# Performance work log

Measured on AMD Instinct MI355X. Metric: run time of the kernel, lower is better.

Reference implementation:

```python
import jax, jax.numpy as jnp
import numpy as np

NUM_EMBEDDINGS = 1024
EMBEDDING_DIM = 64
COMMITMENT_COST = 0.25


def setup_inputs() -> dict:
    key = jax.random.key(0)
    k1, k2 = jax.random.split(key)
    z = jax.random.normal(k1, (16, EMBEDDING_DIM, 64, 64), dtype=jnp.float32)
    # nn.Embedding init: uniform(-1/K, 1/K)
    emb = jax.random.uniform(
        k2, (NUM_EMBEDDINGS, EMBEDDING_DIM), dtype=jnp.float32,
        minval=-1.0 / NUM_EMBEDDINGS, maxval=1.0 / NUM_EMBEDDINGS)
    return {"z": z, "emb": emb}


def reference(z, emb):
    # b c h w -> b h w c
    zc = jnp.transpose(z, (0, 2, 3, 1))
    B, H, W, D = zc.shape
    zf = zc.reshape(-1, D)  # [N, D]
    K = emb.shape[0]

    # L2 distances: ||z||^2 + ||e||^2 - 2 z e^T   -> [N, K]
    distances = (jnp.sum(zf * zf, axis=1, keepdims=True)
                 + jnp.sum(emb * emb, axis=1)
                 - 2.0 * jnp.matmul(zf, emb.T))
    encoding_indices = jnp.argmin(distances, axis=1)  # [N]

    # one_hot @ emb  ==  gather
    quantized = emb[encoding_indices].reshape(zc.shape)  # [B,H,W,D]

    reconstruction_errors = jnp.sum((quantized - zc) ** 2, axis=-1).reshape(-1)
    avg_error = jnp.mean(reconstruction_errors)

    e_latent_loss = jnp.mean((jax.lax.stop_gradient(quantized) - zc) ** 2)
    q_latent_loss = jnp.mean((quantized - jax.lax.stop_gradient(zc)) ** 2)
    loss = q_latent_loss + COMMITMENT_COST * e_latent_loss

    # straight-through estimator
    quantized_st = zc + jax.lax.stop_gradient(quantized - zc)
    out = jnp.transpose(quantized_st, (0, 3, 1, 2))  # b h w c -> b c h w

    # perplexity: avg one-hot usage (histogram instead of dense one-hot)
    N = zf.shape[0]
    counts = jnp.zeros((K,), dtype=jnp.float32).at[encoding_indices].add(1.0)
    avg_probs = counts / N
    perplexity = jnp.exp(-jnp.sum(avg_probs * jnp.log(avg_probs + 1e-10)))

    return out, loss, perplexity, avg_error
```

## Files before the change

### kernel.cpp

```cpp
#include <hip/hip_runtime.h>
#include <stdint.h>

#define HW   4096
#define NEMB 1024

typedef float        f32x4  __attribute__((ext_vector_type(4)));
typedef short        bf16x8 __attribute__((ext_vector_type(8)));
typedef unsigned int u32x4  __attribute__((ext_vector_type(4)));

#define CVTPK(D, LO, HI) asm("v_cvt_pk_bf16_f32 %0, %1, %2" : "=v"(D) : "v"(LO), "v"(HI))

__device__ __forceinline__ void gload_lds16(const float* g, float* l) {
    __builtin_amdgcn_global_load_lds(
        (const __attribute__((address_space(1))) void*)(uintptr_t)g,
        (__attribute__((address_space(3))) void*)(uintptr_t)l, 16, 0, 0);
}

__global__ __launch_bounds__(128) void vq_init(const float* __restrict__ emb,
                                               unsigned int* __restrict__ counts,
                                               float* __restrict__ errsum,
                                               float* __restrict__ ens) {
    const int gid  = blockIdx.x * 128 + threadIdx.x;
    const int k    = gid >> 1;
    const int half = gid & 1;
    if (half == 0) counts[k] = 0u;
    if (gid == 0) *errsum = 0.0f;
    const float* e = emb + k * 64 + half * 32;
    float nrm = 0.0f;
    #pragma unroll
    for (int c = 0; c < 4; ++c) {
        f32x4 v0 = *(const f32x4*)(e + c * 8);
        f32x4 v1 = *(const f32x4*)(e + c * 8 + 4);
        nrm += v0.x*v0.x + v0.y*v0.y + v0.z*v0.z + v0.w*v0.w
             + v1.x*v1.x + v1.y*v1.y + v1.z*v1.z + v1.w*v1.w;
    }
    float o = __shfl_xor(nrm, 1, 64);
    if (half == 0) ens[k] = 1.0f + (nrm + o);
}

__global__ __launch_bounds__(512, 4)
void vq_main(const float* __restrict__ z, const float* __restrict__ emb,
             const float* __restrict__ ens,
             float* __restrict__ out, unsigned int* __restrict__ counts,
             float* __restrict__ errsum)
{
    __shared__ __attribute__((aligned(16))) float z_lds[64 * 128];
    __shared__ __attribute__((aligned(16))) unsigned int et_w[256 * 32];
    __shared__ __attribute__((aligned(16))) float ens_lds[NEMB];
    __shared__ int   idx_sh[128];
    __shared__ float errp[512];

    const int t   = threadIdx.x;
    const int n0  = blockIdx.x * 128;
    const int bb  = n0 >> 12;
    const int hw0 = n0 & 4095;
    const float* zb = z + bb * (64 * HW) + hw0;

    #pragma unroll
    for (int it = 0; it < 4; ++it) {
        const int p = it * 512 + t;
        gload_lds16(zb + (p >> 5) * HW + (p & 31) * 4, z_lds + p * 4);
    }
    if (t < 256) gload_lds16(ens + t * 4, ens_lds + t * 4);

    #pragma unroll
    for (int it = 0; it < 4; ++it) {
        const int q = it * 512 + t;
        const int r = q >> 3, c = q & 7;
        const float* s2 = emb + r * 64 + c * 8;
        f32x4 e0 = *(const f32x4*)s2;
        f32x4 e1 = *(const f32x4*)(s2 + 4);
        u32x4 v;
        CVTPK(v.x, e0.x, e0.y); CVTPK(v.y, e0.z, e0.w);
        CVTPK(v.z, e1.x, e1.y); CVTPK(v.w, e1.z, e1.w);
        *(u32x4*)&et_w[r * 32 + ((c ^ (r & 7)) << 2)] = v;
    }
    __syncthreads();

    const int l   = t & 63;
    const int wv  = t >> 6;
    const int col = l & 15;
    const int bg  = l >> 4;

    bf16x8 a0, a1;
    {
        const int xs = wv * 16 + col;
        u32x4 wa, wb;
        #pragma unroll
        for (int p2 = 0; p2 < 4; ++p2) {
            float lo = z_lds[(bg * 8 + p2 * 2    ) * 128 + xs];
            float hi = z_lds[(bg * 8 + p2 * 2 + 1) * 128 + xs];
            CVTPK(wa[p2], lo, hi);
            float lo2 = z_lds[(32 + bg * 8 + p2 * 2    ) * 128 + xs];
            float hi2 = z_lds[(32 + bg * 8 + p2 * 2 + 1) * 128 + xs];
            CVTPK(wb[p2], lo2, hi2);
        }
        a0 = __builtin_bit_cast(bf16x8, wa);
        a1 = __builtin_bit_cast(bf16x8, wb);
    }

    const int slot0 = bg ^ (col & 7);
    const unsigned int* ep0 = et_w + col * 32 + slot0 * 4;
    const unsigned int* ep1 = et_w + col * 32 + (slot0 ^ 4) * 4;
    const float* ensp = ens_lds + col;

    unsigned int mkey[4] = {~0u, ~0u, ~0u, ~0u};

    #pragma unroll
    for (int kt = 0; kt < 4; ++kt) {
        f32x4 pf[8];
        if (kt < 3) {
            const float* src = emb + (kt + 1) * 256 * 64;
            #pragma unroll
            for (int it = 0; it < 4; ++it) {
                const int q = it * 512 + t;
                const float* s2 = src + (q >> 3) * 64 + (q & 7) * 8;
                pf[it * 2]     = *(const f32x4*)s2;
                pf[it * 2 + 1] = *(const f32x4*)(s2 + 4);
            }
        }

        __builtin_amdgcn_s_setprio(1);
        #pragma unroll
        for (int i = 0; i < 16; ++i) {
            u32x4 bw0 = *(const u32x4*)(ep0 + i * 512);
            u32x4 bw1 = *(const u32x4*)(ep1 + i * 512);
            float en1 = ensp[kt * 256 + i * 16];
            f32x4 cc = {0.0f, 0.0f, 0.0f, 0.0f};
            cc = __builtin_amdgcn_mfma_f32_16x16x32_bf16(a0, __builtin_bit_cast(bf16x8, bw0), cc, 0, 0, 0);
            cc = __builtin_amdgcn_mfma_f32_16x16x32_bf16(a1, __builtin_bit_cast(bf16x8, bw1), cc, 0, 0, 0);
            const unsigned int kg = (unsigned int)(kt * 256 + i * 16 + col);
            #pragma unroll
            for (int j = 0; j < 4; ++j) {
                float s = fmaf(-2.0f, cc[j], en1);
                unsigned int key = (__builtin_bit_cast(unsigned int, s) & 0xFFFFFC00u) | kg;
                mkey[j] = mkey[j] < key ? mkey[j] : key;
            }
        }
        __builtin_amdgcn_s_setprio(0);

        u32x4 vv[4];
        if (kt < 3) {
            #pragma unroll
            for (int it = 0; it < 4; ++it) {
                CVTPK(vv[it].x, pf[it*2].x,   pf[it*2].y);
                CVTPK(vv[it].y, pf[it*2].z,   pf[it*2].w);
                CVTPK(vv[it].z, pf[it*2+1].x, pf[it*2+1].y);
                CVTPK(vv[it].w, pf[it*2+1].z, pf[it*2+1].w);
            }
        }

        __syncthreads();
        if (kt < 3) {
            #pragma unroll
            for (int it = 0; it < 4; ++it) {
                const int q = it * 512 + t;
                const int r = q >> 3, c = q & 7;
                *(u32x4*)&et_w[r * 32 + ((c ^ (r & 7)) << 2)] = vv[it];
            }
            __syncthreads();
        }
    }

    #pragma unroll
    for (int j = 0; j < 4; ++j) {
        #pragma unroll
        for (int m = 1; m <= 8; m <<= 1) {
            unsigned int o = (unsigned int)__shfl_xor((int)mkey[j], m, 64);
            mkey[j] = mkey[j] < o ? mkey[j] : o;
        }
    }
    if (col == 0) {
        #pragma unroll
        for (int j = 0; j < 4; ++j)
            idx_sh[wv * 16 + bg * 4 + j] = (int)(mkey[j] & 1023u);
    }
    __syncthreads();

    if (t < 128) atomicAdd(&counts[idx_sh[t]], 1u);

    {
        const int x  = t & 127;
        const int cg = t >> 7;
        const int idx = idx_sh[x];
        const float* er = emb + idx * 64;
        float* ob = out + bb * (64 * HW) + hw0 + x;
        float part = 0.0f;
        #pragma unroll
        for (int cq = 0; cq < 4; ++cq) {
            const int c = cg * 16 + cq * 4;
            f32x4 e4 = *(const f32x4*)&er[c];
            float z0 = z_lds[(c+0) * 128 + x];
            float z1 = z_lds[(c+1) * 128 + x];
            float z2 = z_lds[(c+2) * 128 + x];
            float z3 = z_lds[(c+3) * 128 + x];
            ob[(c+0) * HW] = z0 + (e4.x - z0);
            ob[(c+1) * HW] = z1 + (e4.y - z1);
            ob[(c+2) * HW] = z2 + (e4.z - z2);
            ob[(c+3) * HW] = z3 + (e4.w - z3);
            float d0 = z0 - e4.x, d1 = z1 - e4.y, d2 = z2 - e4.z, d3 = z3 - e4.w;
            part = fmaf(d0, d0, part); part = fmaf(d1, d1, part);
            part = fmaf(d2, d2, part); part = fmaf(d3, d3, part);
        }
        errp[t] = part;
    }
    __syncthreads();
    if (t < 128) {
        float s = (errp[t] + errp[t + 128]) + (errp[t + 256] + errp[t + 384]);
        #pragma unroll
        for (int off = 32; off >= 1; off >>= 1) s += __shfl_down(s, off, 64);
        if ((t & 63) == 0) atomicAdd(errsum, s);
    }
}

__global__ __launch_bounds__(256) void vq_fin(const unsigned int* __restrict__ counts,
                                              const float* __restrict__ errsum,
                                              float* __restrict__ scal)
{
    __shared__ float part[4];
    const int t = threadIdx.x;
    float s = 0.0f;
    for (int k = t; k < NEMB; k += 256) {
        float p = (float)counts[k] * (1.0f / 65536.0f);
        s += p * logf(p + 1e-10f);
    }
    #pragma unroll
    for (int off = 32; off >= 1; off >>= 1) s += __shfl_down(s, off, 64);
    if ((t & 63) == 0) part[t >> 6] = s;
    __syncthreads();
    if (t == 0) {
        float tot = (part[0] + part[1]) + (part[2] + part[3]);
        float es  = *errsum;
        scal[0] = 1.25f * (es * (1.0f / 4194304.0f));
        scal[1] = expf(-tot);
        scal[2] = es * (1.0f / 65536.0f);
    }
}

extern "C" void kernel_launch(void* const* d_in, const int* in_sizes, int n_in,
                              void* d_out, int out_size, void* d_ws, size_t ws_size,
                              hipStream_t stream) {
    const float* z   = (const float*)d_in[0];
    const float* emb = (const float*)d_in[1];
    float* out = (float*)d_out;
    unsigned int* counts = (unsigned int*)d_ws;
    float* errsum = (float*)((char*)d_ws + 4096);
    float* ens    = (float*)((char*)d_ws + 8192);

    vq_init<<<16, 128, 0, stream>>>(emb, counts, errsum, ens);
    vq_main<<<512, 512, 0, stream>>>(z, emb, ens, out, counts, errsum);
    vq_fin<<<1, 256, 0, stream>>>(counts, errsum, out + 4194304);
}
```

Before: 44.55 us.

## Pre-convert codebook to swizzled bf16 once and stream it via double-buffered LDS DMA

The init kernel now converts the codebook to bf16 once, in the swizzled layout, and writes it to workspace. The main kernel then loads 128-row tiles directly into two LDS buffers with global_load_lds, double-buffered across 8 k-steps. This replaces the per-block fp32 loads, conversions and register-staged stores of all 1024 rows. It also drops one block-wide sync and the LDS stage in the error reduction, so each wave does its own shuffle reduce and atomic. The cost is more syncs per block (8 tile steps instead of 4), more atomics on errsum, and hand-written vmcnt waits that must match the number of outstanding loads.

```diff
diff --git a/kernel.cpp b/kernel.cpp
--- a/kernel.cpp
+++ b/kernel.cpp
@@ -10,7 +10,7 @@
 
 #define CVTPK(D, LO, HI) asm("v_cvt_pk_bf16_f32 %0, %1, %2" : "=v"(D) : "v"(LO), "v"(HI))
 
-__device__ __forceinline__ void gload_lds16(const float* g, float* l) {
+__device__ __forceinline__ void gload_lds16(const void* g, void* l) {
     __builtin_amdgcn_global_load_lds(
         (const __attribute__((address_space(1))) void*)(uintptr_t)g,
         (__attribute__((address_space(3))) void*)(uintptr_t)l, 16, 0, 0);
@@ -19,20 +19,27 @@
 __global__ __launch_bounds__(128) void vq_init(const float* __restrict__ emb,
                                                unsigned int* __restrict__ counts,
                                                float* __restrict__ errsum,
-                                               float* __restrict__ ens) {
+                                               float* __restrict__ ens,
+                                               unsigned int* __restrict__ embw) {
     const int gid  = blockIdx.x * 128 + threadIdx.x;
     const int k    = gid >> 1;
     const int half = gid & 1;
     if (half == 0) counts[k] = 0u;
     if (gid == 0) *errsum = 0.0f;
     const float* e = emb + k * 64 + half * 32;
+    unsigned int* dst = embw + (k >> 7) * 4096 + (k & 127) * 32;
     float nrm = 0.0f;
     #pragma unroll
-    for (int c = 0; c < 4; ++c) {
-        f32x4 v0 = *(const f32x4*)(e + c * 8);
-        f32x4 v1 = *(const f32x4*)(e + c * 8 + 4);
+    for (int ci = 0; ci < 4; ++ci) {
+        const int c = half * 4 + ci;
+        f32x4 v0 = *(const f32x4*)(e + ci * 8);
+        f32x4 v1 = *(const f32x4*)(e + ci * 8 + 4);
         nrm += v0.x*v0.x + v0.y*v0.y + v0.z*v0.z + v0.w*v0.w
              + v1.x*v1.x + v1.y*v1.y + v1.z*v1.z + v1.w*v1.w;
+        u32x4 w;
+        CVTPK(w.x, v0.x, v0.y); CVTPK(w.y, v0.z, v0.w);
+        CVTPK(w.z, v1.x, v1.y); CVTPK(w.w, v1.z, v1.w);
+        *(u32x4*)&dst[(c ^ (k & 7)) << 2] = w;
     }
     float o = __shfl_xor(nrm, 1, 64);
     if (half == 0) ens[k] = 1.0f + (nrm + o);
@@ -40,15 +47,16 @@
 
 __global__ __launch_bounds__(512, 4)
 void vq_main(const float* __restrict__ z, const float* __restrict__ emb,
-             const float* __restrict__ ens,
+             const float* __restrict__ ens, const unsigned int* __restrict__ embw,
              float* __restrict__ out, unsigned int* __restrict__ counts,
              float* __restrict__ errsum)
 {
     __shared__ __attribute__((aligned(16))) float z_lds[64 * 128];
-    __shared__ __attribute__((aligned(16))) unsigned int et_w[256 * 32];
+    __shared__ __attribute__((aligned(16))) unsigned int et0[4096];
+    __shared__ __attribute__((aligned(16))) unsigned int et1[4096];
     __shared__ __attribute__((aligned(16))) float ens_lds[NEMB];
     __shared__ int   idx_sh[128];
-    __shared__ float errp[512];
+    __shared__ float errw[8];
 
     const int t   = threadIdx.x;
     const int n0  = blockIdx.x * 128;
@@ -62,18 +70,15 @@
         gload_lds16(zb + (p >> 5) * HW + (p & 31) * 4, z_lds + p * 4);
     }
     if (t < 256) gload_lds16(ens + t * 4, ens_lds + t * 4);
-
-    #pragma unroll
-    for (int it = 0; it < 4; ++it) {
-        const int q = it * 512 + t;
-        const int r = q >> 3, c = q & 7;
-        const float* s2 = emb + r * 64 + c * 8;
-        f32x4 e0 = *(const f32x4*)s2;
-        f32x4 e1 = *(const f32x4*)(s2 + 4);
-        u32x4 v;
-        CVTPK(v.x, e0.x, e0.y); CVTPK(v.y, e0.z, e0.w);
-        CVTPK(v.z, e1.x, e1.y); CVTPK(v.w, e1.z, e1.w);
-        *(u32x4*)&et_w[r * 32 + ((c ^ (r & 7)) << 2)] = v;
+    #pragma unroll
+    for (int it = 0; it < 2; ++it) {
+        const int p = it * 512 + t;
+        gload_lds16(embw + p * 4, et0 + p * 4);
+    }
+    #pragma unroll
+    for (int it = 0; it < 2; ++it) {
+        const int p = it * 512 + t;
+        gload_lds16(embw + 4096 + p * 4, et1 + p * 4);
     }
     __syncthreads();
 
@@ -99,37 +104,27 @@
         a1 = __builtin_bit_cast(bf16x8, wb);
     }
 
-    const int slot0 = bg ^ (col & 7);
-    const unsigned int* ep0 = et_w + col * 32 + slot0 * 4;
-    const unsigned int* ep1 = et_w + col * 32 + (slot0 ^ 4) * 4;
+    const int slot0 = (bg ^ (col & 7)) << 2;
+    const int rowoff = col * 32;
     const float* ensp = ens_lds + col;
 
     unsigned int mkey[4] = {~0u, ~0u, ~0u, ~0u};
 
-    #pragma unroll
-    for (int kt = 0; kt < 4; ++kt) {
-        f32x4 pf[8];
-        if (kt < 3) {
-            const float* src = emb + (kt + 1) * 256 * 64;
-            #pragma unroll
-            for (int it = 0; it < 4; ++it) {
-                const int q = it * 512 + t;
-                const float* s2 = src + (q >> 3) * 64 + (q & 7) * 8;
-                pf[it * 2]     = *(const f32x4*)s2;
-                pf[it * 2 + 1] = *(const f32x4*)(s2 + 4);
-            }
-        }
-
-        __builtin_amdgcn_s_setprio(1);
-        #pragma unroll
-        for (int i = 0; i < 16; ++i) {
+    #pragma unroll 2
+    for (int kt = 0; kt < 8; ++kt) {
+        const unsigned int* etb = (kt & 1) ? et1 : et0;
+        const unsigned int* ep0 = etb + rowoff + slot0;
+        const unsigned int* ep1 = etb + rowoff + (slot0 ^ 16);
+
+        #pragma unroll
+        for (int i = 0; i < 8; ++i) {
             u32x4 bw0 = *(const u32x4*)(ep0 + i * 512);
             u32x4 bw1 = *(const u32x4*)(ep1 + i * 512);
-            float en1 = ensp[kt * 256 + i * 16];
+            float en1 = ensp[kt * 128 + i * 16];
             f32x4 cc = {0.0f, 0.0f, 0.0f, 0.0f};
             cc = __builtin_amdgcn_mfma_f32_16x16x32_bf16(a0, __builtin_bit_cast(bf16x8, bw0), cc, 0, 0, 0);
             cc = __builtin_amdgcn_mfma_f32_16x16x32_bf16(a1, __builtin_bit_cast(bf16x8, bw1), cc, 0, 0, 0);
-            const unsigned int kg = (unsigned int)(kt * 256 + i * 16 + col);
+            const unsigned int kg = (unsigned int)(kt * 128 + i * 16 + col);
             #pragma unroll
             for (int j = 0; j < 4; ++j) {
                 float s = fmaf(-2.0f, cc[j], en1);
@@ -137,26 +132,20 @@
                 mkey[j] = mkey[j] < key ? mkey[j] : key;
             }
         }
-        __builtin_amdgcn_s_setprio(0);
-
-        u32x4 vv[4];
-        if (kt < 3) {
-            #pragma unroll
-            for (int it = 0; it < 4; ++it) {
-                CVTPK(vv[it].x, pf[it*2].x,   pf[it*2].y);
-                CVTPK(vv[it].y, pf[it*2].z,   pf[it*2].w);
-                CVTPK(vv[it].z, pf[it*2+1].x, pf[it*2+1].y);
-                CVTPK(vv[it].w, pf[it*2+1].z, pf[it*2+1].w);
-            }
-        }
-
-        __syncthreads();
-        if (kt < 3) {
-            #pragma unroll
-            for (int it = 0; it < 4; ++it) {
-                const int q = it * 512 + t;
-                const int r = q >> 3, c = q & 7;
-                *(u32x4*)&et_w[r * 32 + ((c ^ (r & 7)) << 2)] = vv[it];
+
+        if (kt < 7) {
+            __syncthreads();
+            if (kt < 6) {
+                unsigned int* wbuf = (kt & 1) ? et1 : et0;
+                const unsigned int* src = embw + (kt + 2) * 4096;
+                #pragma unroll
+                for (int it = 0; it < 2; ++it) {
+                    const int p = it * 512 + t;
+                    gload_lds16(src + p * 4, wbuf + p * 4);
+                }
+                asm volatile("s_waitcnt vmcnt(2)" ::: "memory");
+            } else {
+                asm volatile("s_waitcnt vmcnt(0)" ::: "memory");
             }
             __syncthreads();
         }
@@ -179,13 +168,13 @@
 
     if (t < 128) atomicAdd(&counts[idx_sh[t]], 1u);
 
+    float part = 0.0f;
     {
         const int x  = t & 127;
         const int cg = t >> 7;
         const int idx = idx_sh[x];
         const float* er = emb + idx * 64;
         float* ob = out + bb * (64 * HW) + hw0 + x;
-        float part = 0.0f;
         #pragma unroll
         for (int cq = 0; cq < 4; ++cq) {
             const int c = cg * 16 + cq * 4;
@@ -202,14 +191,12 @@
             part = fmaf(d0, d0, part); part = fmaf(d1, d1, part);
             part = fmaf(d2, d2, part); part = fmaf(d3, d3, part);
         }
-        errp[t] = part;
-    }
-    __syncthreads();
-    if (t < 128) {
-        float s = (errp[t] + errp[t + 128]) + (errp[t + 256] + errp[t + 384]);
+    }
+    {
+        float s = part;
         #pragma unroll
         for (int off = 32; off >= 1; off >>= 1) s += __shfl_down(s, off, 64);
-        if ((t & 63) == 0) atomicAdd(errsum, s);
+        if (l == 0) atomicAdd(errsum, s);
     }
 }
 
@@ -246,8 +233,9 @@
     unsigned int* counts = (unsigned int*)d_ws;
     float* errsum = (float*)((char*)d_ws + 4096);
     float* ens    = (float*)((char*)d_ws + 8192);
-
-    vq_init<<<16, 128, 0, stream>>>(emb, counts, errsum, ens);
-    vq_main<<<512, 512, 0, stream>>>(z, emb, ens, out, counts, errsum);
+    unsigned int* embw = (unsigned int*)((char*)d_ws + 16384);
+
+    vq_init<<<16, 128, 0, stream>>>(emb, counts, errsum, ens, embw);
+    vq_main<<<512, 512, 0, stream>>>(z, emb, ens, embw, out, counts, errsum);
     vq_fin<<<1, 256, 0, stream>>>(counts, errsum, out + 4194304);
 }
```

New measurement: 79.97 us. +79.5%, slower.
